# Kernel tuning notes

Measured on AMD Instinct MI355X. Metric: run time of the kernel, lower is better.

Reference implementation:

```python
import jax, jax.numpy as jnp
import numpy as np

ALPHA = 0.25
GAMMA = 2.0


def setup_inputs() -> dict:
    key = jax.random.key(0)
    k1, k2 = jax.random.split(key)
    B, T = 4096, 4096
    inputs = jax.random.normal(k1, (B, T, 2), dtype=jnp.float32)
    targets = jax.random.randint(k2, (B, T), 0, 2, dtype=jnp.int64)
    return {"inputs": inputs, "targets": targets}


def reference(inputs, targets):
    # one-hot targets: ts[i, j, targets[i, j]] = 1  -> [B, T, 2]
    ts = jax.nn.one_hot(targets, 2, dtype=inputs.dtype)
    x = inputs
    # binary_cross_entropy_with_logits, reduction='none' (numerically stable)
    bce = jnp.maximum(x, 0.0) - x * ts + jnp.log1p(jnp.exp(-jnp.abs(x)))
    a = 2.0 * ALPHA - 1.0
    b = 1.0 - ALPHA
    at = ts * a + b
    pt = jnp.exp(-bce)
    f_loss = at * (1.0 - pt) ** GAMMA * bce
    return jnp.mean(f_loss)
```

## Files before the change

kernel.cpp:

```cpp
#include <hip/hip_runtime.h>


constexpr unsigned NPOS    = 4096u * 4096u;
constexpr int      BLOCKS  = 2048;
constexpr int      THREADS = 256;
constexpr unsigned NQUAD   = NPOS / 4;
constexpr unsigned STRIDE  = (unsigned)BLOCKS * THREADS;
constexpr int      ITERS   = (int)(NQUAD / STRIDE);

__device__ __forceinline__ float g_of(float z) {
    float e   = __expf(-z);
    float u   = 1.f + e;
    float pt  = __builtin_amdgcn_rcpf(u);
    float bce = __logf(u);
    float om  = e * pt;
    return om * om * bce;
}

__global__ __launch_bounds__(THREADS, 4) void focal_partial(
    const float4* __restrict__ in,
    const int4*   __restrict__ tgt,
    float*        __restrict__ partial)
{
    const unsigned tid = blockIdx.x * (unsigned)THREADS + threadIdx.x;

    float acc_t = 0.f;
    float acc_f = 0.f;

#pragma unroll
    for (int i = 0; i < ITERS; ++i) {
        unsigned q  = tid + (unsigned)i * STRIDE;
        float4   v0 = in[2u * q];
        float4   v1 = in[2u * q + 1u];
        int4     t4 = tgt[q];

        float x0[4] = {v0.x, v0.z, v1.x, v1.z};
        float x1[4] = {v0.y, v0.w, v1.y, v1.w};
        int   tt[4] = {t4.x, t4.y, t4.z, t4.w};

#pragma unroll
        for (int p = 0; p < 4; ++p) {
            bool  one = tt[p] != 0;
            float xt  = one ? x1[p] : x0[p];
            float xf  = one ? x0[p] : x1[p];
            acc_t += g_of(xt);
            acc_f += g_of(-xf);
        }
    }

    float acc = 0.25f * acc_t + 0.75f * acc_f;

#pragma unroll
    for (int off = 32; off > 0; off >>= 1)
        acc += __shfl_down(acc, off, 64);

    __shared__ float sm[THREADS / 64];
    const int lane = threadIdx.x & 63;
    const int wid  = threadIdx.x >> 6;
    if (lane == 0) sm[wid] = acc;
    __syncthreads();
    if (threadIdx.x == 0) {
        float s = 0.f;
#pragma unroll
        for (int w = 0; w < THREADS / 64; ++w) s += sm[w];
        partial[blockIdx.x] = s;
    }
}

__global__ __launch_bounds__(256) void focal_final(
    const float* __restrict__ partial, float* __restrict__ out)
{
    float acc = 0.f;
    for (int i = threadIdx.x; i < BLOCKS; i += 256) acc += partial[i];
#pragma unroll
    for (int off = 32; off > 0; off >>= 1)
        acc += __shfl_down(acc, off, 64);

    __shared__ float sm[4];
    const int lane = threadIdx.x & 63;
    const int wid  = threadIdx.x >> 6;
    if (lane == 0) sm[wid] = acc;
    __syncthreads();
    if (threadIdx.x == 0) {
        float s = sm[0] + sm[1] + sm[2] + sm[3];
        out[0] = s * (1.0f / (2.0f * (float)NPOS));
    }
}

extern "C" void kernel_launch(void* const* d_in, const int* in_sizes, int n_in,
                              void* d_out, int out_size, void* d_ws, size_t ws_size,
                              hipStream_t stream) {
    const float4* in  = (const float4*)d_in[0];
    const int4*   tgt = (const int4*)d_in[1];
    float* partial    = (float*)d_ws;
    float* out        = (float*)d_out;

    focal_partial<<<BLOCKS, THREADS, 0, stream>>>(in, tgt, partial);
    focal_final<<<1, 256, 0, stream>>>(partial, out);
}
```

Baseline: 38.91 us.

## Fuse final reduction via last-block atomic counter and batch loads per group

Replaces the separate final-reduction kernel with a last-block-done pattern: each block writes its partial, bumps an atomic counter, and the last block sums all partials. Loads are restructured so each thread reads one float4 and one int2 per step, with eight steps' loads issued before compute to raise memory-level parallelism. This removes one kernel launch but adds a memset launch and a fence-plus-atomic per block. Targets are read as int2, which assumes they arrive as 32-bit ints, the same assumption the previous int4 reads made.

```diff
diff --git a/kernel.cpp b/kernel.cpp
--- a/kernel.cpp
+++ b/kernel.cpp
@@ -4,9 +4,10 @@
 constexpr unsigned NPOS    = 4096u * 4096u;
 constexpr int      BLOCKS  = 2048;
 constexpr int      THREADS = 256;
-constexpr unsigned NQUAD   = NPOS / 4;
+constexpr unsigned NF4     = NPOS / 2;
 constexpr unsigned STRIDE  = (unsigned)BLOCKS * THREADS;
-constexpr int      ITERS   = (int)(NQUAD / STRIDE);
+constexpr int      ITERS   = (int)(NF4 / STRIDE);
+constexpr int      GROUP   = 8;
 
 __device__ __forceinline__ float g_of(float z) {
     float e   = __expf(-z);
@@ -17,10 +18,12 @@
     return om * om * bce;
 }
 
-__global__ __launch_bounds__(THREADS, 4) void focal_partial(
-    const float4* __restrict__ in,
-    const int4*   __restrict__ tgt,
-    float*        __restrict__ partial)
+__global__ __launch_bounds__(THREADS, 4) void focal_fused(
+    const float4* __restrict__ in4,
+    const int2*   __restrict__ tg2,
+    float*        __restrict__ partial,
+    unsigned*     __restrict__ cnt,
+    float*        __restrict__ out)
 {
     const unsigned tid = blockIdx.x * (unsigned)THREADS + threadIdx.x;
 
@@ -28,23 +31,31 @@
     float acc_f = 0.f;
 
 #pragma unroll
-    for (int i = 0; i < ITERS; ++i) {
-        unsigned q  = tid + (unsigned)i * STRIDE;
-        float4   v0 = in[2u * q];
-        float4   v1 = in[2u * q + 1u];
-        int4     t4 = tgt[q];
-
-        float x0[4] = {v0.x, v0.z, v1.x, v1.z};
-        float x1[4] = {v0.y, v0.w, v1.y, v1.w};
-        int   tt[4] = {t4.x, t4.y, t4.z, t4.w};
-
+    for (int grp = 0; grp < ITERS / GROUP; ++grp) {
+        float4 v[GROUP];
+        int2   t[GROUP];
 #pragma unroll
-        for (int p = 0; p < 4; ++p) {
-            bool  one = tt[p] != 0;
-            float xt  = one ? x1[p] : x0[p];
-            float xf  = one ? x0[p] : x1[p];
-            acc_t += g_of(xt);
-            acc_f += g_of(-xf);
+        for (int j = 0; j < GROUP; ++j) {
+            unsigned idx = (unsigned)(grp * GROUP + j) * STRIDE + tid;
+            v[j] = in4[idx];
+            t[j] = tg2[idx];
+        }
+#pragma unroll
+        for (int j = 0; j < GROUP; ++j) {
+            {
+                bool  one = t[j].x != 0;
+                float xt  = one ? v[j].y : v[j].x;
+                float xf  = one ? v[j].x : v[j].y;
+                acc_t += g_of(xt);
+                acc_f += g_of(-xf);
+            }
+            {
+                bool  one = t[j].y != 0;
+                float xt  = one ? v[j].w : v[j].z;
+                float xf  = one ? v[j].z : v[j].w;
+                acc_t += g_of(xt);
+                acc_f += g_of(-xf);
+            }
         }
     }
 
@@ -55,46 +66,49 @@
         acc += __shfl_down(acc, off, 64);
 
     __shared__ float sm[THREADS / 64];
+    __shared__ bool  amLast;
     const int lane = threadIdx.x & 63;
     const int wid  = threadIdx.x >> 6;
     if (lane == 0) sm[wid] = acc;
     __syncthreads();
+
     if (threadIdx.x == 0) {
         float s = 0.f;
 #pragma unroll
         for (int w = 0; w < THREADS / 64; ++w) s += sm[w];
         partial[blockIdx.x] = s;
+        __threadfence();
+        unsigned old = atomicAdd(cnt, 1u);
+        amLast = (old == (unsigned)(BLOCKS - 1));
     }
-}
+    __syncthreads();
 
-__global__ __launch_bounds__(256) void focal_final(
-    const float* __restrict__ partial, float* __restrict__ out)
-{
-    float acc = 0.f;
-    for (int i = threadIdx.x; i < BLOCKS; i += 256) acc += partial[i];
+    if (amLast) {
+        __threadfence();
+        float s = 0.f;
+        for (int i = threadIdx.x; i < BLOCKS; i += THREADS)
+            s += partial[i];
 #pragma unroll
-    for (int off = 32; off > 0; off >>= 1)
-        acc += __shfl_down(acc, off, 64);
-
-    __shared__ float sm[4];
-    const int lane = threadIdx.x & 63;
-    const int wid  = threadIdx.x >> 6;
-    if (lane == 0) sm[wid] = acc;
-    __syncthreads();
-    if (threadIdx.x == 0) {
-        float s = sm[0] + sm[1] + sm[2] + sm[3];
-        out[0] = s * (1.0f / (2.0f * (float)NPOS));
+        for (int off = 32; off > 0; off >>= 1)
+            s += __shfl_down(s, off, 64);
+        if (lane == 0) sm[wid] = s;
+        __syncthreads();
+        if (threadIdx.x == 0) {
+            float tot = sm[0] + sm[1] + sm[2] + sm[3];
+            out[0] = tot * (1.0f / (2.0f * (float)NPOS));
+        }
     }
 }
 
 extern "C" void kernel_launch(void* const* d_in, const int* in_sizes, int n_in,
                               void* d_out, int out_size, void* d_ws, size_t ws_size,
                               hipStream_t stream) {
-    const float4* in  = (const float4*)d_in[0];
-    const int4*   tgt = (const int4*)d_in[1];
-    float* partial    = (float*)d_ws;
-    float* out        = (float*)d_out;
+    const float4* in4 = (const float4*)d_in[0];
+    const int2*   tg2 = (const int2*)d_in[1];
+    float*    partial = (float*)d_ws;
+    unsigned* cnt     = (unsigned*)((char*)d_ws + BLOCKS * sizeof(float));
+    float*    out     = (float*)d_out;
 
-    focal_partial<<<BLOCKS, THREADS, 0, stream>>>(in, tgt, partial);
-    focal_final<<<1, 256, 0, stream>>>(partial, out);
+    hipMemsetAsync(cnt, 0, sizeof(unsigned), stream);
+    focal_fused<<<BLOCKS, THREADS, 0, stream>>>(in4, tg2, partial, cnt, out);
 }
```

Measured after the change: 108.1 us. 178% more time.

## Issue all loads upfront with per-thread float4/int2 granularity

Applied to the files above, without the earlier changes.

Each thread now handles one float4 of logits (two positions) and one int2 of targets per iteration, so adjacent lanes touch contiguous 16-byte and 8-byte chunks instead of strided pairs of float4 plus an int4. All loads for the thread are issued into register arrays before any math, with a sched_barrier that stops the compiler from interleaving them, to maximise memory-level parallelism. The cost is more registers and smaller target loads per instruction. The targets are treated as 32-bit ints, as in the original code.

```diff
diff --git a/kernel.cpp b/kernel.cpp
--- a/kernel.cpp
+++ b/kernel.cpp
@@ -4,9 +4,9 @@
 constexpr unsigned NPOS    = 4096u * 4096u;
 constexpr int      BLOCKS  = 2048;
 constexpr int      THREADS = 256;
-constexpr unsigned NQUAD   = NPOS / 4;
+constexpr unsigned NF4     = NPOS / 2;
 constexpr unsigned STRIDE  = (unsigned)BLOCKS * THREADS;
-constexpr int      ITERS   = (int)(NQUAD / STRIDE);
+constexpr int      ITERS   = (int)(NF4 / STRIDE);
 
 __device__ __forceinline__ float g_of(float z) {
     float e   = __expf(-z);
@@ -18,31 +18,37 @@
 }
 
 __global__ __launch_bounds__(THREADS, 4) void focal_partial(
-    const float4* __restrict__ in,
-    const int4*   __restrict__ tgt,
+    const float4* __restrict__ in4,
+    const int2*   __restrict__ tg2,
     float*        __restrict__ partial)
 {
     const unsigned tid = blockIdx.x * (unsigned)THREADS + threadIdx.x;
 
+    float4 v[ITERS];
+    int2   t[ITERS];
+#pragma unroll
+    for (int i = 0; i < ITERS; ++i) {
+        unsigned idx = (unsigned)i * STRIDE + tid;
+        v[i] = in4[idx];
+        t[i] = tg2[idx];
+    }
+    __builtin_amdgcn_sched_barrier(0);
+
     float acc_t = 0.f;
     float acc_f = 0.f;
-
 #pragma unroll
     for (int i = 0; i < ITERS; ++i) {
-        unsigned q  = tid + (unsigned)i * STRIDE;
-        float4   v0 = in[2u * q];
-        float4   v1 = in[2u * q + 1u];
-        int4     t4 = tgt[q];
-
-        float x0[4] = {v0.x, v0.z, v1.x, v1.z};
-        float x1[4] = {v0.y, v0.w, v1.y, v1.w};
-        int   tt[4] = {t4.x, t4.y, t4.z, t4.w};
-
-#pragma unroll
-        for (int p = 0; p < 4; ++p) {
-            bool  one = tt[p] != 0;
-            float xt  = one ? x1[p] : x0[p];
-            float xf  = one ? x0[p] : x1[p];
+        {
+            bool  one = t[i].x != 0;
+            float xt  = one ? v[i].y : v[i].x;
+            float xf  = one ? v[i].x : v[i].y;
+            acc_t += g_of(xt);
+            acc_f += g_of(-xf);
+        }
+        {
+            bool  one = t[i].y != 0;
+            float xt  = one ? v[i].w : v[i].z;
+            float xf  = one ? v[i].z : v[i].w;
             acc_t += g_of(xt);
             acc_f += g_of(-xf);
         }
@@ -90,11 +96,11 @@
 extern "C" void kernel_launch(void* const* d_in, const int* in_sizes, int n_in,
                               void* d_out, int out_size, void* d_ws, size_t ws_size,
                               hipStream_t stream) {
-    const float4* in  = (const float4*)d_in[0];
-    const int4*   tgt = (const int4*)d_in[1];
+    const float4* in4 = (const float4*)d_in[0];
+    const int2*   tg2 = (const int2*)d_in[1];
     float* partial    = (float*)d_ws;
     float* out        = (float*)d_out;
 
-    focal_partial<<<BLOCKS, THREADS, 0, stream>>>(in, tgt, partial);
+    focal_partial<<<BLOCKS, THREADS, 0, stream>>>(in4, tg2, partial);
     focal_final<<<1, 256, 0, stream>>>(partial, out);
 }
```

Result: slower. 42.32 us (+8.8%).
